# Optimization experiments

Hardware: AMD Instinct MI355X
Metric: run time of the kernel (lower is better)

## Reference

```python
import jax, jax.numpy as jnp
import numpy as np

N = 100000
E = 1600000
NFEAT, NHID1, NHID2, NCLASS, NSTRUC = 512, 256, 128, 40, 128


def glorot(key, shape):
    lim = 1.0 / np.sqrt(shape[0])
    return jax.random.uniform(key, shape, jnp.float32, -lim, lim)


def setup_inputs() -> dict:
    key = jax.random.key(0)
    ks = jax.random.split(key, 12)
    x = jax.random.normal(ks[0], (N, NFEAT), jnp.float32)
    edge_index = jax.random.randint(ks[1], (2, E), 0, N, jnp.int32)
    edge_weight = jax.random.uniform(ks[2], (E,), jnp.float32)
    return {
        "x": x,
        "edge_index": edge_index,
        "edge_weight": edge_weight,
        "W1": glorot(ks[3], (NFEAT, NHID1)), "b1": jnp.zeros((NHID1,), jnp.float32),
        "W2": glorot(ks[4], (NHID1, NHID2)), "b2": jnp.zeros((NHID2,), jnp.float32),
        "W3": glorot(ks[5], (NHID2, NCLASS)), "b3": jnp.zeros((NCLASS,), jnp.float32),
        "We": glorot(ks[6], (NHID1, NSTRUC)), "be": jnp.zeros((NSTRUC,), jnp.float32),
    }


def spmm(edge_index, edge_weight, support):
    # adj @ support with adj given as weighted edge list (dst <- src)
    src, dst = edge_index[0], edge_index[1]
    msgs = support[src] * edge_weight[:, None]  # [E, d]
    return jax.ops.segment_sum(msgs, dst, num_segments=N)


def gc_layer(x, edge_index, edge_weight, W, b):
    support = x @ W
    return spmm(edge_index, edge_weight, support) + b


def reference(x, edge_index, edge_weight, W1, b1, W2, b2, W3, b3, We, be):
    # eval mode: dropout is identity
    h = jax.nn.relu(gc_layer(x, edge_index, edge_weight, W1, b1))
    out1 = jax.nn.relu(gc_layer(h, edge_index, edge_weight, W2, b2))
    out1 = gc_layer(out1, edge_index, edge_weight, W3, b3)
    out2 = h @ We + be
    return jax.nn.log_softmax(out1, axis=1), out2
```

## Files before the change

kernel.cpp:

```cpp
#include <hip/hip_runtime.h>
#include <hip/hip_bf16.h>

#define NNODES 100000
#define NEDGES 1600000
#define BSH 7
#define NBUCK ((NNODES + 127) >> 7)

typedef __attribute__((ext_vector_type(8))) short bf16x8;
typedef __attribute__((ext_vector_type(4))) short bf16x4;
typedef __attribute__((ext_vector_type(2))) short bf16x2;
typedef __attribute__((ext_vector_type(4))) float f32x4;
typedef __attribute__((ext_vector_type(2))) float f32x2;

static __device__ __forceinline__ short f2bf(float f) {
  __hip_bfloat16 b = __float2bfloat16(f);
  return __builtin_bit_cast(short, b);
}
static __device__ __forceinline__ float bf2f(short s) {
  unsigned int u = ((unsigned int)(unsigned short)s) << 16;
  return __builtin_bit_cast(float, u);
}
static __device__ __forceinline__ void fma4(f32x4& a, float w, bf16x4 v) {
  a[0] = fmaf(w, bf2f(v[0]), a[0]);
  a[1] = fmaf(w, bf2f(v[1]), a[1]);
  a[2] = fmaf(w, bf2f(v[2]), a[2]);
  a[3] = fmaf(w, bf2f(v[3]), a[3]);
}
static __device__ __forceinline__ void fma2(f32x2& a, float w, bf16x2 v) {
  a[0] = fmaf(w, bf2f(v[0]), a[0]);
  a[1] = fmaf(w, bf2f(v[1]), a[1]);
}

__global__ void wtrans_kernel(const float* __restrict__ W, short* __restrict__ Wt,
                              int K, int Nvalid, int Npad) {
  int idx = blockIdx.x * blockDim.x + threadIdx.x;
  if (idx >= Npad * K) return;
  int n = idx / K, k = idx - n * K;
  Wt[idx] = (n < Nvalid) ? f2bf(W[(size_t)k * Nvalid + n]) : (short)0;
}

__global__ void bcount_kernel(const int* __restrict__ ei, int* __restrict__ bcnt) {
  __shared__ int h[NBUCK];
  for (int i = threadIdx.x; i < NBUCK; i += 256) h[i] = 0;
  __syncthreads();
  int stride = gridDim.x * 256;
  for (int e = blockIdx.x * 256 + threadIdx.x; e < NEDGES; e += stride)
    atomicAdd(&h[ei[NEDGES + e] >> BSH], 1);
  __syncthreads();
  for (int i = threadIdx.x; i < NBUCK; i += 256)
    if (h[i]) atomicAdd(&bcnt[i], h[i]);
}

__global__ void bscan_kernel(const int* __restrict__ bcnt, int* __restrict__ bbase,
                             int* __restrict__ bcur, int* __restrict__ rowptr) {
  __shared__ int lds[1024];
  int t = threadIdx.x;
  int c = (t < NBUCK) ? bcnt[t] : 0;
  lds[t] = c;
  __syncthreads();
  for (int off = 1; off < 1024; off <<= 1) {
    int v = (t >= off) ? lds[t - off] : 0;
    __syncthreads();
    lds[t] += v;
    __syncthreads();
  }
  if (t < NBUCK) {
    int ex = lds[t] - c;
    bbase[t] = ex;
    bcur[t] = ex;
  }
  if (t == NBUCK) bbase[t] = NEDGES;
  if (t == 0) rowptr[NNODES] = NEDGES;
}

#define P4CHUNK 8192
__global__ void bscatter_kernel(const int* __restrict__ ei, const float* __restrict__ ew,
                                int* __restrict__ bcur, int2* __restrict__ tmp) {
  __shared__ int cnt[NBUCK];
  __shared__ int pos[NBUCK];
  int tid = threadIdx.x;
  for (int i = tid; i < NBUCK; i += 256) cnt[i] = 0;
  __syncthreads();
  int base = blockIdx.x * P4CHUNK;
  int end = base + P4CHUNK;
  if (end > NEDGES) end = NEDGES;
  for (int e = base + tid; e < end; e += 256)
    atomicAdd(&cnt[ei[NEDGES + e] >> BSH], 1);
  __syncthreads();
  for (int i = tid; i < NBUCK; i += 256)
    if (cnt[i]) pos[i] = atomicAdd(&bcur[i], cnt[i]);
  __syncthreads();
  for (int e = base + tid; e < end; e += 256) {
    int d = ei[NEDGES + e];
    int b = d >> BSH;
    int p = atomicAdd(&pos[b], 1);
    tmp[p] = make_int2(ei[e] | ((d & 127) << 17), __float_as_int(ew[e]));
  }
}

__global__ void bsort_kernel(const int* __restrict__ bbase, const int2* __restrict__ tmp,
                             int2* __restrict__ edat, int* __restrict__ rowptr) {
  __shared__ int hist[128];
  __shared__ int cur[128];
  int b = blockIdx.x;
  int tid = threadIdx.x;
  int base = bbase[b], cnt = bbase[b + 1] - base;
  if (tid < 128) hist[tid] = 0;
  __syncthreads();
  for (int i = tid; i < cnt; i += 256)
    atomicAdd(&hist[(tmp[base + i].x >> 17) & 127], 1);
  __syncthreads();
  int c = (tid < 128) ? hist[tid] : 0;
  if (tid < 128) cur[tid] = c;
  __syncthreads();
  for (int off = 1; off < 128; off <<= 1) {
    int v = (tid < 128 && tid >= off) ? cur[tid - off] : 0;
    __syncthreads();
    if (tid < 128) cur[tid] += v;
    __syncthreads();
  }
  if (tid < 128) {
    int ex = cur[tid] - c;
    int node = (b << BSH) + tid;
    if (node < NNODES) rowptr[node] = base + ex;
    cur[tid] = base + ex;
  }
  __syncthreads();
  for (int i = tid; i < cnt; i += 256) {
    int2 r = tmp[base + i];
    int d = (r.x >> 17) & 127;
    int p = atomicAdd(&cur[d], 1);
    edat[p] = make_int2(r.x & 0x1FFFF, r.y);
  }
}

#define LDSTR 72
template <bool AF32, int EPI>
__launch_bounds__(256, 2)
__global__ void gemm_tiled(const void* __restrict__ Aptr, int K,
                           const short* __restrict__ Wt,
                           void* __restrict__ Cp0, float* __restrict__ Cp1,
                           const float* __restrict__ bias, int nvalid, int ldc) {
  __shared__ __align__(16) short As[128 * LDSTR];
  __shared__ __align__(16) short Bs[128 * LDSTR];
  int tid = threadIdx.x;
  int lane = tid & 63, wv = tid >> 6;
  int wr = wv >> 1, wc = wv & 1;
  int m0 = blockIdx.y * 128;
  int n0 = blockIdx.x * 128;
  f32x4 acc[4][4];
#pragma unroll
  for (int i = 0; i < 4; i++)
#pragma unroll
    for (int j = 0; j < 4; j++) acc[i][j] = (f32x4){0.f, 0.f, 0.f, 0.f};

  int srow = tid >> 3;
  int scol = (tid & 7) * 8;

  for (int k0 = 0; k0 < K; k0 += 64) {
#pragma unroll
    for (int p = 0; p < 4; p++) {
      int ml = p * 32 + srow;
      int arow = m0 + ml;
      if (arow >= NNODES) arow = NNODES - 1;
      bf16x8 av;
      if (AF32) {
        const float* ap = (const float*)Aptr + (size_t)arow * K + k0 + scol;
        f32x4 a0 = *(const f32x4*)ap;
        f32x4 a1 = *(const f32x4*)(ap + 4);
#pragma unroll
        for (int j = 0; j < 4; j++) { av[j] = f2bf(a0[j]); av[4 + j] = f2bf(a1[j]); }
      } else {
        av = *(const bf16x8*)((const short*)Aptr + (size_t)arow * K + k0 + scol);
      }
      *(bf16x8*)&As[ml * LDSTR + scol] = av;
      bf16x8 bv = *(const bf16x8*)(Wt + (size_t)(n0 + ml) * K + k0 + scol);
      *(bf16x8*)&Bs[ml * LDSTR + scol] = bv;
    }
    __syncthreads();
    int r = lane & 15, quad = lane >> 4;
#pragma unroll
    for (int kk = 0; kk < 64; kk += 32) {
      bf16x8 af[4], bfr[4];
#pragma unroll
      for (int i = 0; i < 4; i++)
        af[i] = *(const bf16x8*)&As[(wr * 64 + i * 16 + r) * LDSTR + kk + quad * 8];
#pragma unroll
      for (int j = 0; j < 4; j++)
        bfr[j] = *(const bf16x8*)&Bs[(wc * 64 + j * 16 + r) * LDSTR + kk + quad * 8];
#pragma unroll
      for (int i = 0; i < 4; i++)
#pragma unroll
        for (int j = 0; j < 4; j++)
          acc[i][j] = __builtin_amdgcn_mfma_f32_16x16x32_bf16(af[i], bfr[j], acc[i][j], 0, 0, 0);
    }
    __syncthreads();
  }

  int quad = lane >> 4, cl = lane & 15;
#pragma unroll
  for (int i = 0; i < 4; i++) {
    int rowb = m0 + wr * 64 + i * 16 + quad * 4;
#pragma unroll
    for (int rr = 0; rr < 4; rr++) {
      int row = rowb + rr;
      if (row < NNODES) {
#pragma unroll
        for (int j = 0; j < 4; j++) {
          int col = n0 + wc * 64 + j * 16 + cl;
          float v = acc[i][j][rr];
          if (EPI == 0) {
            ((short*)Cp0)[(size_t)row * ldc + col] = f2bf(v);
          } else if (EPI == 1) {
            if (col < nvalid) Cp1[(size_t)row * nvalid + col] = v;
          } else {
            if (col < 128) ((short*)Cp0)[(size_t)row * 128 + col] = f2bf(v);
            else Cp1[(size_t)row * 128 + (col - 128)] = v + bias[col - 128];
          }
        }
      }
    }
  }
}

__global__ void spmm1_kernel(const int* __restrict__ rowptr, const int2* __restrict__ edat,
                             const short* __restrict__ S,
                             const float* __restrict__ bias, short* __restrict__ H) {
  int node = blockIdx.x * 4 + (threadIdx.x >> 6);
  if (node >= NNODES) return;
  int lane = threadIdx.x & 63;
  int c0 = lane * 4;
  const short* Sc = S + c0;
  f32x4 acc0 = (f32x4){0.f, 0.f, 0.f, 0.f};
  f32x4 acc1 = (f32x4){0.f, 0.f, 0.f, 0.f};
  int beg = rowptr[node], end = rowptr[node + 1];
  int i = beg;
  for (; i + 8 <= end; i += 8) {
    int2 e[8];
    bf16x4 v[8];
#pragma unroll
    for (int j = 0; j < 8; j++) e[j] = edat[i + j];
#pragma unroll
    for (int j = 0; j < 8; j++) v[j] = *(const bf16x4*)(Sc + (size_t)e[j].x * 256);
#pragma unroll
    for (int j = 0; j < 8; j++) {
      float w = __int_as_float(e[j].y);
      if (j & 1) fma4(acc1, w, v[j]); else fma4(acc0, w, v[j]);
    }
  }
  for (; i < end; i++) {
    int2 e = edat[i];
    fma4(acc0, __int_as_float(e.y), *(const bf16x4*)(Sc + (size_t)e.x * 256));
  }
  f32x4 a;
  a[0] = acc0[0] + acc1[0]; a[1] = acc0[1] + acc1[1];
  a[2] = acc0[2] + acc1[2]; a[3] = acc0[3] + acc1[3];
  f32x4 b = *(const f32x4*)(bias + c0);
  bf16x4 h;
#pragma unroll
  for (int j = 0; j < 4; j++) h[j] = f2bf(fmaxf(a[j] + b[j], 0.f));
  *(bf16x4*)(H + (size_t)node * 256 + c0) = h;
}

__global__ void spmm2_kernel(const int* __restrict__ rowptr, const int2* __restrict__ edat,
                             const short* __restrict__ S,
                             const float* __restrict__ bias, short* __restrict__ H) {
  int node = blockIdx.x * 4 + (threadIdx.x >> 6);
  if (node >= NNODES) return;
  int lane = threadIdx.x & 63;
  int c0 = lane * 2;
  const short* Sc = S + c0;
  f32x2 acc0 = (f32x2){0.f, 0.f};
  f32x2 acc1 = (f32x2){0.f, 0.f};
  int beg = rowptr[node], end = rowptr[node + 1];
  int i = beg;
  for (; i + 8 <= end; i += 8) {
    int2 e[8];
    bf16x2 v[8];
#pragma unroll
    for (int j = 0; j < 8; j++) e[j] = edat[i + j];
#pragma unroll
    for (int j = 0; j < 8; j++) v[j] = *(const bf16x2*)(Sc + (size_t)e[j].x * 128);
#pragma unroll
    for (int j = 0; j < 8; j++) {
      float w = __int_as_float(e[j].y);
      if (j & 1) fma2(acc1, w, v[j]); else fma2(acc0, w, v[j]);
    }
  }
  for (; i < end; i++) {
    int2 e = edat[i];
    fma2(acc0, __int_as_float(e.y), *(const bf16x2*)(Sc + (size_t)e.x * 128));
  }
  float a0 = acc0[0] + acc1[0], a1 = acc0[1] + acc1[1];
  bf16x2 h;
  h[0] = f2bf(fmaxf(a0 + bias[c0 + 0], 0.f));
  h[1] = f2bf(fmaxf(a1 + bias[c0 + 1], 0.f));
  *(bf16x2*)(H + (size_t)node * 128 + c0) = h;
}

__global__ void spmm3_kernel(const int* __restrict__ rowptr, const int2* __restrict__ edat,
                             const float* __restrict__ S3,
                             const float* __restrict__ b3, float* __restrict__ out1) {
  int node = blockIdx.x * 4 + (threadIdx.x >> 6);
  if (node >= NNODES) return;
  int lane = threadIdx.x & 63;
  bool act = lane < 40;
  float acc0 = 0.f, acc1 = 0.f;
  int beg = rowptr[node], end = rowptr[node + 1];
  if (act) {
    int i = beg;
    for (; i + 8 <= end; i += 8) {
      int2 e[8];
      float v[8];
#pragma unroll
      for (int j = 0; j < 8; j++) e[j] = edat[i + j];
#pragma unroll
      for (int j = 0; j < 8; j++) v[j] = S3[(size_t)e[j].x * 40 + lane];
#pragma unroll
      for (int j = 0; j < 8; j++) {
        float w = __int_as_float(e[j].y);
        if (j & 1) acc1 = fmaf(w, v[j], acc1); else acc0 = fmaf(w, v[j], acc0);
      }
    }
    for (; i < end; i++) {
      int2 e = edat[i];
      acc0 = fmaf(__int_as_float(e.y), S3[(size_t)e.x * 40 + lane], acc0);
    }
  }
  float acc = acc0 + acc1;
  if (act) acc += b3[lane];
  float v = act ? acc : -__builtin_inff();
  for (int off = 32; off > 0; off >>= 1) v = fmaxf(v, __shfl_xor(v, off));
  float e = act ? expf(acc - v) : 0.f;
  for (int off = 32; off > 0; off >>= 1) e += __shfl_xor(e, off);
  float ls = logf(e);
  if (act) out1[(size_t)node * 40 + lane] = acc - v - ls;
}

extern "C" void kernel_launch(void* const* d_in, const int* in_sizes, int n_in,
                              void* d_out, int out_size, void* d_ws, size_t ws_size,
                              hipStream_t stream) {
  const float* x  = (const float*)d_in[0];
  const int*   ei = (const int*)d_in[1];
  const float* ew = (const float*)d_in[2];
  const float* W1 = (const float*)d_in[3];
  const float* b1 = (const float*)d_in[4];
  const float* W2 = (const float*)d_in[5];
  const float* b2 = (const float*)d_in[6];
  const float* W3 = (const float*)d_in[7];
  const float* b3 = (const float*)d_in[8];
  const float* We = (const float*)d_in[9];
  const float* be = (const float*)d_in[10];
  float* out1 = (float*)d_out;
  float* out2 = (float*)d_out + (size_t)NNODES * 40;

  char* w = (char*)d_ws;
  size_t off = 0;
  auto alloc = [&](size_t bytes) -> char* {
    char* p = w + off;
    off += (bytes + 255) & ~(size_t)255;
    return p;
  };
  int*   rowptr = (int*)alloc((size_t)(NNODES + 1) * 4);
  int*   bcnt   = (int*)alloc((size_t)NBUCK * 4);
  int*   bbase  = (int*)alloc((size_t)(NBUCK + 1) * 4);
  int*   bcur   = (int*)alloc((size_t)NBUCK * 4);
  int2*  edat   = (int2*)alloc((size_t)NEDGES * 8);
  short* Wt1    = (short*)alloc((size_t)256 * 512 * 2);
  short* Wt2e   = (short*)alloc((size_t)256 * 256 * 2);
  short* Wt3    = (short*)alloc((size_t)128 * 128 * 2);
  short* S1bf   = (short*)alloc((size_t)NNODES * 256 * 2);
  short* Hbf    = (short*)alloc((size_t)NNODES * 256 * 2);
  short* S2bf   = (short*)alloc((size_t)NNODES * 128 * 2);
  short* Tbf    = (short*)alloc((size_t)NNODES * 128 * 2);
  float* S3     = (float*)alloc((size_t)NNODES * 40 * 4);
  int2*  tmp    = (int2*)S3;

  hipMemsetAsync(bcnt, 0, (size_t)NBUCK * 4, stream);
  bcount_kernel<<<256, 256, 0, stream>>>(ei, bcnt);
  bscan_kernel<<<1, 1024, 0, stream>>>(bcnt, bbase, bcur, rowptr);
  bscatter_kernel<<<(NEDGES + P4CHUNK - 1) / P4CHUNK, 256, 0, stream>>>(ei, ew, bcur, tmp);
  bsort_kernel<<<NBUCK, 256, 0, stream>>>(bbase, tmp, edat, rowptr);

  wtrans_kernel<<<(256 * 512 + 255) / 256, 256, 0, stream>>>(W1, Wt1, 512, 256, 256);
  wtrans_kernel<<<(128 * 256 + 255) / 256, 256, 0, stream>>>(W2, Wt2e, 256, 128, 128);
  wtrans_kernel<<<(128 * 256 + 255) / 256, 256, 0, stream>>>(We, Wt2e + (size_t)128 * 256, 256, 128, 128);
  wtrans_kernel<<<(128 * 128 + 255) / 256, 256, 0, stream>>>(W3, Wt3, 128, 40, 128);

  int gblocks = (NNODES + 127) / 128;
  int sblocks = (NNODES + 3) / 4;

  gemm_tiled<true, 0><<<dim3(2, gblocks), 256, 0, stream>>>(x, 512, Wt1, S1bf, nullptr, nullptr, 256, 256);
  spmm1_kernel<<<sblocks, 256, 0, stream>>>(rowptr, edat, S1bf, b1, Hbf);
  gemm_tiled<false, 2><<<dim3(2, gblocks), 256, 0, stream>>>(Hbf, 256, Wt2e, S2bf, out2, be, 256, 128);
  spmm2_kernel<<<sblocks, 256, 0, stream>>>(rowptr, edat, S2bf, b2, Tbf);
  gemm_tiled<false, 1><<<dim3(1, gblocks), 256, 0, stream>>>(Tbf, 128, Wt3, nullptr, S3, nullptr, 40, 40);
  spmm3_kernel<<<sblocks, 256, 0, stream>>>(rowptr, edat, S3, b3, out1);
}
```

Baseline: 788.4 us.

## Load edge chunks wave-cooperatively and broadcast via readlane in persistent SpMM kernels

The three SpMM kernels become grid-stride persistent kernels (fixed grid of 1536 blocks) that walk nodes per wavefront. Each wave loads up to 64 edges at once, one per lane, and broadcasts source and weight with readlane instead of every lane re-reading the same edge records. Gathers are issued in groups of 16 (or 8 for the tail), padding the partial group with zero-weight edges to node 0. The S3 buffer gets slack so those padded reads stay in bounds. This trades redundant edge loads and per-node launch overhead for some wasted padded gathers and scalar broadcast work.

```diff
diff --git a/kernel.cpp b/kernel.cpp
--- a/kernel.cpp
+++ b/kernel.cpp
@@ -5,6 +5,7 @@
 #define NEDGES 1600000
 #define BSH 7
 #define NBUCK ((NNODES + 127) >> 7)
+#define SPBLK 1536
 
 typedef __attribute__((ext_vector_type(8))) short bf16x8;
 typedef __attribute__((ext_vector_type(4))) short bf16x4;
@@ -223,118 +224,157 @@
   }
 }
 
+
+template <int NE>
+static __device__ __forceinline__ void gat1(int2 me, int b, const short* Sc,
+                                            f32x4& acc0, f32x4& acc1) {
+  int src[NE]; float wt[NE]; bf16x4 v[NE];
+#pragma unroll
+  for (int j = 0; j < NE; j++) {
+    src[j] = __builtin_amdgcn_readlane(me.x, b + j);
+    wt[j] = __builtin_bit_cast(float, __builtin_amdgcn_readlane(me.y, b + j));
+  }
+#pragma unroll
+  for (int j = 0; j < NE; j++) v[j] = *(const bf16x4*)(Sc + (size_t)src[j] * 256);
+#pragma unroll
+  for (int j = 0; j < NE; j++) {
+    if (j & 1) fma4(acc1, wt[j], v[j]); else fma4(acc0, wt[j], v[j]);
+  }
+}
+
+template <int NE>
+static __device__ __forceinline__ void gat2(int2 me, int b, const short* Sc,
+                                            f32x2& acc0, f32x2& acc1) {
+  int src[NE]; float wt[NE]; bf16x2 v[NE];
+#pragma unroll
+  for (int j = 0; j < NE; j++) {
+    src[j] = __builtin_amdgcn_readlane(me.x, b + j);
+    wt[j] = __builtin_bit_cast(float, __builtin_amdgcn_readlane(me.y, b + j));
+  }
+#pragma unroll
+  for (int j = 0; j < NE; j++) v[j] = *(const bf16x2*)(Sc + (size_t)src[j] * 128);
+#pragma unroll
+  for (int j = 0; j < NE; j++) {
+    if (j & 1) fma2(acc1, wt[j], v[j]); else fma2(acc0, wt[j], v[j]);
+  }
+}
+
+template <int NE>
+static __device__ __forceinline__ void gat3(int2 me, int b, const float* S3l,
+                                            float& acc0, float& acc1) {
+  int src[NE]; float wt[NE]; float v[NE];
+#pragma unroll
+  for (int j = 0; j < NE; j++) {
+    src[j] = __builtin_amdgcn_readlane(me.x, b + j);
+    wt[j] = __builtin_bit_cast(float, __builtin_amdgcn_readlane(me.y, b + j));
+  }
+#pragma unroll
+  for (int j = 0; j < NE; j++) v[j] = S3l[(size_t)src[j] * 40];
+#pragma unroll
+  for (int j = 0; j < NE; j++) {
+    if (j & 1) acc1 = fmaf(wt[j], v[j], acc1); else acc0 = fmaf(wt[j], v[j], acc0);
+  }
+}
+
+__launch_bounds__(256, 6)
 __global__ void spmm1_kernel(const int* __restrict__ rowptr, const int2* __restrict__ edat,
                              const short* __restrict__ S,
                              const float* __restrict__ bias, short* __restrict__ H) {
-  int node = blockIdx.x * 4 + (threadIdx.x >> 6);
-  if (node >= NNODES) return;
+  int nw = gridDim.x * 4;
+  int wid = blockIdx.x * 4 + (threadIdx.x >> 6);
   int lane = threadIdx.x & 63;
   int c0 = lane * 4;
   const short* Sc = S + c0;
-  f32x4 acc0 = (f32x4){0.f, 0.f, 0.f, 0.f};
-  f32x4 acc1 = (f32x4){0.f, 0.f, 0.f, 0.f};
-  int beg = rowptr[node], end = rowptr[node + 1];
-  int i = beg;
-  for (; i + 8 <= end; i += 8) {
-    int2 e[8];
-    bf16x4 v[8];
-#pragma unroll
-    for (int j = 0; j < 8; j++) e[j] = edat[i + j];
-#pragma unroll
-    for (int j = 0; j < 8; j++) v[j] = *(const bf16x4*)(Sc + (size_t)e[j].x * 256);
-#pragma unroll
-    for (int j = 0; j < 8; j++) {
-      float w = __int_as_float(e[j].y);
-      if (j & 1) fma4(acc1, w, v[j]); else fma4(acc0, w, v[j]);
-    }
-  }
-  for (; i < end; i++) {
-    int2 e = edat[i];
-    fma4(acc0, __int_as_float(e.y), *(const bf16x4*)(Sc + (size_t)e.x * 256));
-  }
-  f32x4 a;
-  a[0] = acc0[0] + acc1[0]; a[1] = acc0[1] + acc1[1];
-  a[2] = acc0[2] + acc1[2]; a[3] = acc0[3] + acc1[3];
-  f32x4 b = *(const f32x4*)(bias + c0);
-  bf16x4 h;
-#pragma unroll
-  for (int j = 0; j < 4; j++) h[j] = f2bf(fmaxf(a[j] + b[j], 0.f));
-  *(bf16x4*)(H + (size_t)node * 256 + c0) = h;
-}
-
+  f32x4 bv = *(const f32x4*)(bias + c0);
+  for (int node = wid; node < NNODES; node += nw) {
+    f32x4 acc0 = (f32x4){0.f, 0.f, 0.f, 0.f};
+    f32x4 acc1 = (f32x4){0.f, 0.f, 0.f, 0.f};
+    int beg = rowptr[node], end = rowptr[node + 1];
+    for (int w0 = beg; w0 < end; w0 += 64) {
+      int wcnt = end - w0;
+      if (wcnt > 64) wcnt = 64;
+      int2 me = (lane < wcnt) ? edat[w0 + lane] : make_int2(0, 0);
+      int g16 = wcnt >> 4, rem = wcnt & 15;
+      int b = 0;
+      for (int g = 0; g < g16; ++g, b += 16) gat1<16>(me, b, Sc, acc0, acc1);
+      if (rem) {
+        if (rem > 8) gat1<16>(me, b, Sc, acc0, acc1);
+        else gat1<8>(me, b, Sc, acc0, acc1);
+      }
+    }
+    bf16x4 h;
+#pragma unroll
+    for (int j = 0; j < 4; j++) h[j] = f2bf(fmaxf(acc0[j] + acc1[j] + bv[j], 0.f));
+    *(bf16x4*)(H + (size_t)node * 256 + c0) = h;
+  }
+}
+
+__launch_bounds__(256, 6)
 __global__ void spmm2_kernel(const int* __restrict__ rowptr, const int2* __restrict__ edat,
                              const short* __restrict__ S,
                              const float* __restrict__ bias, short* __restrict__ H) {
-  int node = blockIdx.x * 4 + (threadIdx.x >> 6);
-  if (node >= NNODES) return;
+  int nw = gridDim.x * 4;
+  int wid = blockIdx.x * 4 + (threadIdx.x >> 6);
   int lane = threadIdx.x & 63;
   int c0 = lane * 2;
   const short* Sc = S + c0;
-  f32x2 acc0 = (f32x2){0.f, 0.f};
-  f32x2 acc1 = (f32x2){0.f, 0.f};
-  int beg = rowptr[node], end = rowptr[node + 1];
-  int i = beg;
-  for (; i + 8 <= end; i += 8) {
-    int2 e[8];
-    bf16x2 v[8];
-#pragma unroll
-    for (int j = 0; j < 8; j++) e[j] = edat[i + j];
-#pragma unroll
-    for (int j = 0; j < 8; j++) v[j] = *(const bf16x2*)(Sc + (size_t)e[j].x * 128);
-#pragma unroll
-    for (int j = 0; j < 8; j++) {
-      float w = __int_as_float(e[j].y);
-      if (j & 1) fma2(acc1, w, v[j]); else fma2(acc0, w, v[j]);
-    }
-  }
-  for (; i < end; i++) {
-    int2 e = edat[i];
-    fma2(acc0, __int_as_float(e.y), *(const bf16x2*)(Sc + (size_t)e.x * 128));
-  }
-  float a0 = acc0[0] + acc1[0], a1 = acc0[1] + acc1[1];
-  bf16x2 h;
-  h[0] = f2bf(fmaxf(a0 + bias[c0 + 0], 0.f));
-  h[1] = f2bf(fmaxf(a1 + bias[c0 + 1], 0.f));
-  *(bf16x2*)(H + (size_t)node * 128 + c0) = h;
-}
-
+  float b0 = bias[c0], b1 = bias[c0 + 1];
+  for (int node = wid; node < NNODES; node += nw) {
+    f32x2 acc0 = (f32x2){0.f, 0.f};
+    f32x2 acc1 = (f32x2){0.f, 0.f};
+    int beg = rowptr[node], end = rowptr[node + 1];
+    for (int w0 = beg; w0 < end; w0 += 64) {
+      int wcnt = end - w0;
+      if (wcnt > 64) wcnt = 64;
+      int2 me = (lane < wcnt) ? edat[w0 + lane] : make_int2(0, 0);
+      int g16 = wcnt >> 4, rem = wcnt & 15;
+      int b = 0;
+      for (int g = 0; g < g16; ++g, b += 16) gat2<16>(me, b, Sc, acc0, acc1);
+      if (rem) {
+        if (rem > 8) gat2<16>(me, b, Sc, acc0, acc1);
+        else gat2<8>(me, b, Sc, acc0, acc1);
+      }
+    }
+    bf16x2 h;
+    h[0] = f2bf(fmaxf(acc0[0] + acc1[0] + b0, 0.f));
+    h[1] = f2bf(fmaxf(acc0[1] + acc1[1] + b1, 0.f));
+    *(bf16x2*)(H + (size_t)node * 128 + c0) = h;
+  }
+}
+
+__launch_bounds__(256, 6)
 __global__ void spmm3_kernel(const int* __restrict__ rowptr, const int2* __restrict__ edat,
                              const float* __restrict__ S3,
                              const float* __restrict__ b3, float* __restrict__ out1) {
-  int node = blockIdx.x * 4 + (threadIdx.x >> 6);
-  if (node >= NNODES) return;
+  int nw = gridDim.x * 4;
+  int wid = blockIdx.x * 4 + (threadIdx.x >> 6);
   int lane = threadIdx.x & 63;
   bool act = lane < 40;
-  float acc0 = 0.f, acc1 = 0.f;
-  int beg = rowptr[node], end = rowptr[node + 1];
-  if (act) {
-    int i = beg;
-    for (; i + 8 <= end; i += 8) {
-      int2 e[8];
-      float v[8];
-#pragma unroll
-      for (int j = 0; j < 8; j++) e[j] = edat[i + j];
-#pragma unroll
-      for (int j = 0; j < 8; j++) v[j] = S3[(size_t)e[j].x * 40 + lane];
-#pragma unroll
-      for (int j = 0; j < 8; j++) {
-        float w = __int_as_float(e[j].y);
-        if (j & 1) acc1 = fmaf(w, v[j], acc1); else acc0 = fmaf(w, v[j], acc0);
+  const float* S3l = S3 + lane;
+  float bl = act ? b3[lane] : 0.f;
+  for (int node = wid; node < NNODES; node += nw) {
+    float acc0 = 0.f, acc1 = 0.f;
+    int beg = rowptr[node], end = rowptr[node + 1];
+    for (int w0 = beg; w0 < end; w0 += 64) {
+      int wcnt = end - w0;
+      if (wcnt > 64) wcnt = 64;
+      int2 me = (lane < wcnt) ? edat[w0 + lane] : make_int2(0, 0);
+      int g16 = wcnt >> 4, rem = wcnt & 15;
+      int b = 0;
+      for (int g = 0; g < g16; ++g, b += 16) gat3<16>(me, b, S3l, acc0, acc1);
+      if (rem) {
+        if (rem > 8) gat3<16>(me, b, S3l, acc0, acc1);
+        else gat3<8>(me, b, S3l, acc0, acc1);
       }
     }
-    for (; i < end; i++) {
-      int2 e = edat[i];
-      acc0 = fmaf(__int_as_float(e.y), S3[(size_t)e.x * 40 + lane], acc0);
-    }
-  }
-  float acc = acc0 + acc1;
-  if (act) acc += b3[lane];
-  float v = act ? acc : -__builtin_inff();
-  for (int off = 32; off > 0; off >>= 1) v = fmaxf(v, __shfl_xor(v, off));
-  float e = act ? expf(acc - v) : 0.f;
-  for (int off = 32; off > 0; off >>= 1) e += __shfl_xor(e, off);
-  float ls = logf(e);
-  if (act) out1[(size_t)node * 40 + lane] = acc - v - ls;
+    float acc = acc0 + acc1 + bl;
+    float v = act ? acc : -__builtin_inff();
+    for (int off = 32; off > 0; off >>= 1) v = fmaxf(v, __shfl_xor(v, off));
+    float e = act ? expf(acc - v) : 0.f;
+    for (int off = 32; off > 0; off >>= 1) e += __shfl_xor(e, off);
+    float ls = logf(e);
+    if (act) out1[(size_t)node * 40 + lane] = acc - v - ls;
+  }
 }
 
 extern "C" void kernel_launch(void* const* d_in, const int* in_sizes, int n_in,
@@ -373,7 +413,7 @@
   short* Hbf    = (short*)alloc((size_t)NNODES * 256 * 2);
   short* S2bf   = (short*)alloc((size_t)NNODES * 128 * 2);
   short* Tbf    = (short*)alloc((size_t)NNODES * 128 * 2);
-  float* S3     = (float*)alloc((size_t)NNODES * 40 * 4);
+  float* S3     = (float*)alloc(((size_t)NNODES * 40 + 64) * 4);
   int2*  tmp    = (int2*)S3;
 
   hipMemsetAsync(bcnt, 0, (size_t)NBUCK * 4, stream);
@@ -388,12 +428,11 @@
   wtrans_kernel<<<(128 * 128 + 255) / 256, 256, 0, stream>>>(W3, Wt3, 128, 40, 128);
 
   int gblocks = (NNODES + 127) / 128;
-  int sblocks = (NNODES + 3) / 4;
 
   gemm_tiled<true, 0><<<dim3(2, gblocks), 256, 0, stream>>>(x, 512, Wt1, S1bf, nullptr, nullptr, 256, 256);
-  spmm1_kernel<<<sblocks, 256, 0, stream>>>(rowptr, edat, S1bf, b1, Hbf);
+  spmm1_kernel<<<SPBLK, 256, 0, stream>>>(rowptr, edat, S1bf, b1, Hbf);
   gemm_tiled<false, 2><<<dim3(2, gblocks), 256, 0, stream>>>(Hbf, 256, Wt2e, S2bf, out2, be, 256, 128);
-  spmm2_kernel<<<sblocks, 256, 0, stream>>>(rowptr, edat, S2bf, b2, Tbf);
+  spmm2_kernel<<<SPBLK, 256, 0, stream>>>(rowptr, edat, S2bf, b2, Tbf);
   gemm_tiled<false, 1><<<dim3(1, gblocks), 256, 0, stream>>>(Tbf, 128, Wt3, nullptr, S3, nullptr, 40, 40);
-  spmm3_kernel<<<sblocks, 256, 0, stream>>>(rowptr, edat, S3, b3, out1);
-}
+  spmm3_kernel<<<SPBLK, 256, 0, stream>>>(rowptr, edat, S3, b3, out1);
+}
```

Result: faster. 757.7 us (-3.9%).
